# Kernel optimization log

Hardware: AMD Instinct MI355X
Metric: run time of the kernel (lower is better)

The kernel has to match this reference:

```python
import jax, jax.numpy as jnp
import numpy as np

B, H, W, C = 2, 64, 64, 96
DIN, NST, RNK, K = 192, 16, 6, 4
L = H * W


def _make_ids():
    idx = np.arange(L).reshape(H, W)
    p0 = idx.reshape(-1)
    p1 = idx.T.reshape(-1)
    p2 = p0[::-1].copy()
    p3 = p1[::-1].copy()
    scan = np.stack([p0, p1, p2, p3]).astype(np.int32)
    inv = np.stack([np.argsort(p) for p in scan]).astype(np.int32)
    return jnp.asarray(scan), jnp.asarray(inv)


def setup_inputs() -> dict:
    key = jax.random.key(0)
    ks = jax.random.split(key, 10)
    scan_ids, inv_ids = _make_ids()
    std = RNK ** -0.5
    # dt bias init: inverse-softplus of dt ~ LogUniform(1e-3, 1e-1), as in VMM.dt_init
    u = jax.random.uniform(ks[5], (K, DIN))
    dt = jnp.exp(u * (np.log(0.1) - np.log(0.001)) + np.log(0.001))
    dt_b = dt + jnp.log(-jnp.expm1(-dt))
    return {
        "x": jax.random.normal(ks[0], (B, H, W, C), jnp.float32),
        "W_in": jax.random.normal(ks[1], (2 * DIN, C), jnp.float32) * 0.02,
        "conv_w": jax.random.normal(ks[2], (DIN, 1, 3, 3), jnp.float32) * 0.1,
        "conv_b": jnp.zeros((DIN,), jnp.float32),
        "x_proj_w": jax.random.normal(ks[3], (K, RNK + 2 * NST, DIN), jnp.float32) * 0.02,
        "dt_w": jax.random.uniform(ks[4], (K, DIN, RNK), jnp.float32, -std, std),
        "dt_b": dt_b.astype(jnp.float32),
        "A_logs": jnp.log(jnp.tile(jnp.arange(1, NST + 1, dtype=jnp.float32)[None], (K * DIN, 1))),
        "Ds": jnp.ones((K * DIN,), jnp.float32),
        "gate_w": jax.random.normal(ks[6], (4 * DIN, 4), jnp.float32) * 0.1,  # grouped 1x1 conv, groups=DIN
        "gate_b": jnp.zeros((4 * DIN,), jnp.float32),
        "ln_g": jnp.ones((DIN,), jnp.float32),
        "ln_b": jnp.zeros((DIN,), jnp.float32),
        "W_out": jax.random.normal(ks[7], (C, DIN), jnp.float32) * 0.02,
        "scan_ids": scan_ids,
        "inv_ids": inv_ids,
    }


def _forward(x, W_in, conv_w, conv_b, x_proj_w, dt_w, dt_b, A_logs, Ds, gate_w, gate_b, ln_g, ln_b, W_out, scan_ids, inv_ids):
    b, h, w, c = x.shape
    l = h * w
    din = conv_w.shape[0]
    k = x_proj_w.shape[0]
    nst = A_logs.shape[1]
    rnk = dt_w.shape[2]
    # in_proj + split into x / gate z
    xz = x @ W_in.T
    xc, z = jnp.split(xz, 2, axis=-1)
    xc = jnp.transpose(xc, (0, 3, 1, 2))  # (b, din, h, w)
    # depthwise 3x3 conv + SiLU
    xc = jax.lax.conv_general_dilated(
        xc, conv_w, (1, 1), "SAME", feature_group_count=din,
        dimension_numbers=("NCHW", "OIHW", "NCHW")) + conv_b[None, :, None, None]
    xc = jax.nn.silu(xc)
    # multi-directional gather (mair_ids_scan)
    xf = xc.reshape(b, din, l)
    xs = jnp.moveaxis(xf[:, :, scan_ids], 2, 1)  # (b, k, din, l)
    # x_proj (grouped 1x1 conv) -> dt, B, C
    x_dbl = jnp.einsum("bkdl,krd->bkrl", xs, x_proj_w)
    dts, Bs, Cs = jnp.split(x_dbl, [rnk, rnk + nst], axis=2)  # (b,k,rnk,l),(b,k,n,l),(b,k,n,l)
    delta = jax.nn.softplus(jnp.einsum("bkrl,kdr->bkdl", dts, dt_w) + dt_b[None, :, :, None])
    A = -jnp.exp(A_logs).reshape(k, din, nst)
    dA = jnp.exp(delta[..., None] * A[None, :, :, None, :])              # (b,k,d,l,n)
    dBu = (delta * xs)[..., None] * jnp.moveaxis(Bs, 2, 3)[:, :, None]   # (b,k,d,l,n)

    def step(hst, inp):
        da, dbu = inp
        hst = da * hst + dbu
        return hst, hst

    h0 = jnp.zeros((b, k, din, nst), jnp.float32)
    _, hs = jax.lax.scan(step, h0, (jnp.moveaxis(dA, 3, 0), jnp.moveaxis(dBu, 3, 0)))  # (l,b,k,d,n)
    ys = jnp.einsum("lbkdn,bknl->bkdl", hs, Cs) + xs * Ds.reshape(k, din)[None, :, :, None]
    # inverse scatter (mair_ids_inverse) + concat along channels
    y = jax.vmap(lambda yk, ik: yk[..., ik], in_axes=(1, 0), out_axes=1)(ys, inv_ids)
    y = y.reshape(b, k * din, h, w)
    # ShuffleAttn gating: group = din, group_channels = k
    shuf = y.reshape(b, k, din, h, w).transpose(0, 2, 1, 3, 4).reshape(b, k * din, h, w)
    pooled = shuf.mean(axis=(2, 3)).reshape(b, din, k)
    gate = jax.nn.sigmoid(jnp.einsum("bgi,goi->bgo", pooled, gate_w.reshape(din, k, k)) + gate_b.reshape(din, k))
    gate = gate.transpose(0, 2, 1).reshape(b, k * din)  # channel_rearrange
    y = y * gate[:, :, None, None]
    # sum the 4 direction branches
    y = y.reshape(b, k, din, h, w).sum(axis=1)
    y = jnp.transpose(y, (0, 2, 3, 1))  # (b,h,w,din)
    # LayerNorm(d_inner)
    mu = y.mean(-1, keepdims=True)
    var = ((y - mu) ** 2).mean(-1, keepdims=True)
    y = (y - mu) / jnp.sqrt(var + 1e-5) * ln_g + ln_b
    y = y * jax.nn.silu(z)
    return y @ W_out.T


def reference(x, W_in, conv_w, conv_b, x_proj_w, dt_w, dt_b, A_logs, Ds, gate_w, gate_b, ln_g, ln_b, W_out, scan_ids, inv_ids):
    return _forward(x, W_in, conv_w, conv_b, x_proj_w, dt_w, dt_b, A_logs, Ds, gate_w, gate_b, ln_g, ln_b, W_out, scan_ids, inv_ids)
```

## Files before the change

kernel.cpp:

```cpp
#include <hip/hip_runtime.h>
#include <math.h>

#define BB 2
#define CC 96
#define DIN 192
#define NST 16
#define RNK 6
#define KK 4
#define LL 4096
#define RTOT (RNK + 2*NST)


__global__ __launch_bounds__(256) void k_inproj(const float* __restrict__ x,
        const float* __restrict__ W_in, float* __restrict__ xc_pre,
        float* __restrict__ z_silu) {
    __shared__ float lx[96*65];
    __shared__ float wt[48*196];
    int b = blockIdx.y;
    int l0 = blockIdx.x * 64;
    int t = threadIdx.x;
    for (int i = 0; i < 6; ++i) {
        int e4 = t + 256*i;
        int c4 = e4 % 24, l = e4 / 24;
        float4 v = *(const float4*)&x[((size_t)(b*LL + l0 + l))*96 + 4*c4];
        lx[(4*c4+0)*65 + l] = v.x;
        lx[(4*c4+1)*65 + l] = v.y;
        lx[(4*c4+2)*65 + l] = v.z;
        lx[(4*c4+3)*65 + l] = v.w;
    }
    int lg = t & 15;
    int og = t >> 4;
    for (int z = 0; z < 2; ++z) {
        float acc[4][12];
        #pragma unroll
        for (int j = 0; j < 4; ++j)
            #pragma unroll
            for (int q = 0; q < 12; ++q) acc[j][q] = 0.f;
        for (int p = 0; p < 2; ++p) {
            __syncthreads();
            for (int i = 0; i < 9; ++i) {
                int e4 = t + 256*i;
                int cc4 = e4 % 12, oc = e4 / 12;
                float4 v = *(const float4*)&W_in[((size_t)(z*192 + oc))*96 + p*48 + 4*cc4];
                wt[(4*cc4+0)*196 + oc] = v.x;
                wt[(4*cc4+1)*196 + oc] = v.y;
                wt[(4*cc4+2)*196 + oc] = v.z;
                wt[(4*cc4+3)*196 + oc] = v.w;
            }
            __syncthreads();
            #pragma unroll 2
            for (int cc = 0; cc < 48; ++cc) {
                int c = p*48 + cc;
                float x0 = lx[c*65 + 4*lg + 0];
                float x1 = lx[c*65 + 4*lg + 1];
                float x2 = lx[c*65 + 4*lg + 2];
                float x3 = lx[c*65 + 4*lg + 3];
                const float* wr = &wt[cc*196 + 12*og];
                float4 w0 = *(const float4*)(wr);
                float4 w1 = *(const float4*)(wr + 4);
                float4 w2 = *(const float4*)(wr + 8);
                float wv[12] = {w0.x,w0.y,w0.z,w0.w, w1.x,w1.y,w1.z,w1.w,
                                w2.x,w2.y,w2.z,w2.w};
                #pragma unroll
                for (int q = 0; q < 12; ++q) {
                    acc[0][q] += x0*wv[q];
                    acc[1][q] += x1*wv[q];
                    acc[2][q] += x2*wv[q];
                    acc[3][q] += x3*wv[q];
                }
            }
        }
        float* dst = (z == 0) ? xc_pre : z_silu;
        #pragma unroll
        for (int j = 0; j < 4; ++j) {
            int l = l0 + 4*lg + j;
            size_t base = (size_t)(b*LL + l)*DIN + 12*og;
            float v[12];
            #pragma unroll
            for (int q = 0; q < 12; ++q) {
                float a = acc[j][q];
                v[q] = z ? a/(1.f + __expf(-a)) : a;
            }
            *(float4*)&dst[base]     = make_float4(v[0],v[1],v[2],v[3]);
            *(float4*)&dst[base + 4] = make_float4(v[4],v[5],v[6],v[7]);
            *(float4*)&dst[base + 8] = make_float4(v[8],v[9],v[10],v[11]);
        }
    }
}

__global__ __launch_bounds__(256) void k_conv(const float* __restrict__ xc,
        const float* __restrict__ cw, const float* __restrict__ cb,
        float* __restrict__ out) {
    int gid = blockIdx.x*256 + threadIdx.x;
    int dq = gid % 48;
    int r = gid / 48;
    int l = r & 4095, b = r >> 12;
    int w = l & 63, h = l >> 6;
    int d0 = dq*4;
    float4 acc = *(const float4*)&cb[d0];
    float wreg[4][9];
    #pragma unroll
    for (int j = 0; j < 4; ++j)
        #pragma unroll
        for (int tp = 0; tp < 9; ++tp) wreg[j][tp] = cw[(d0+j)*9 + tp];
    #pragma unroll
    for (int dh = -1; dh <= 1; ++dh) {
        int h2 = h + dh;
        bool okh = (h2 >= 0) && (h2 < 64);
        #pragma unroll
        for (int dw = -1; dw <= 1; ++dw) {
            int w2 = w + dw;
            if (okh && w2 >= 0 && w2 < 64) {
                float4 v = *(const float4*)&xc[((size_t)(b*LL + h2*64 + w2))*DIN + d0];
                int tp = (dh+1)*3 + (dw+1);
                acc.x += v.x*wreg[0][tp];
                acc.y += v.y*wreg[1][tp];
                acc.z += v.z*wreg[2][tp];
                acc.w += v.w*wreg[3][tp];
            }
        }
    }
    float4 o;
    o.x = acc.x/(1.f + __expf(-acc.x));
    o.y = acc.y/(1.f + __expf(-acc.y));
    o.z = acc.z/(1.f + __expf(-acc.z));
    o.w = acc.w/(1.f + __expf(-acc.w));
    *(float4*)&out[((size_t)(b*LL + l))*DIN + d0] = o;
}

__global__ __launch_bounds__(512) void k_proj(const float* __restrict__ xconv,
        const int* __restrict__ scan_ids, const float* __restrict__ xpw,
        float* __restrict__ dts, float* __restrict__ Bs, float* __restrict__ Cs) {
    __shared__ float lxs[96*65];
    __shared__ float lw[RTOT*96];
    __shared__ float lbc[64*33];
    __shared__ int lsid[64];
    int k = blockIdx.y, b = blockIdx.z;
    int l0 = blockIdx.x * 64;
    int t = threadIdx.x;
    if (t < 64) lsid[t] = scan_ids[k*LL + l0 + t];
    int l = t & 63;
    int rg = __builtin_amdgcn_readfirstlane(t >> 6);
    float acc[5];
    #pragma unroll
    for (int j = 0; j < 5; ++j) acc[j] = 0.f;
    for (int p = 0; p < 2; ++p) {
        __syncthreads();
        for (int i = 0; i < 3; ++i) {
            int e4 = t + 512*i;
            int dd4 = e4 % 24, ll = e4 / 24;
            float4 v = *(const float4*)&xconv[((size_t)(b*LL + lsid[ll]))*DIN + p*96 + 4*dd4];
            lxs[(4*dd4+0)*65 + ll] = v.x;
            lxs[(4*dd4+1)*65 + ll] = v.y;
            lxs[(4*dd4+2)*65 + ll] = v.z;
            lxs[(4*dd4+3)*65 + ll] = v.w;
        }
        for (int i = 0; i < 2; ++i) {
            int e4 = t + 512*i;
            if (e4 < RTOT*24) {
                int r = e4 / 24, dd4 = e4 % 24;
                *(float4*)&lw[r*96 + 4*dd4] =
                    *(const float4*)&xpw[(size_t)k*RTOT*DIN + r*DIN + p*96 + 4*dd4];
            }
        }
        __syncthreads();
        for (int dd = 0; dd < 96; dd += 4) {
            float x0 = lxs[(dd+0)*65 + l];
            float x1 = lxs[(dd+1)*65 + l];
            float x2 = lxs[(dd+2)*65 + l];
            float x3 = lxs[(dd+3)*65 + l];
            #pragma unroll
            for (int j = 0; j < 5; ++j) {
                int r = rg + 8*j;
                if (r < RTOT) {
                    float4 w = *(const float4*)&lw[r*96 + dd];
                    acc[j] += x0*w.x + x1*w.y + x2*w.z + x3*w.w;
                }
            }
        }
    }
    int bk = b*KK + k;
    #pragma unroll
    for (int j = 0; j < 5; ++j) {
        int r = rg + 8*j;
        if (r < RNK)       dts[((size_t)bk*LL + l0 + l)*8 + r] = acc[j];
        else if (r < RTOT) lbc[l*33 + (r - RNK)] = acc[j];
    }
    __syncthreads();
    size_t rowb = ((size_t)bk*LL + l0)*NST;
    for (int i = 0; i < 2; ++i) {
        int e = t + 512*i;
        int n = e & 15, ll = e >> 4;
        Bs[rowb + ll*NST + n] = lbc[ll*33 + n];
        Cs[rowb + ll*NST + n] = lbc[ll*33 + 16 + n];
    }
}

__global__ __launch_bounds__(384) void k_scan1(const float* __restrict__ xconv,
        const float* __restrict__ Bs, const float* __restrict__ Cs,
        const float* __restrict__ dts, const float* __restrict__ dtw,
        const float* __restrict__ dtb,
        const int* __restrict__ scan_ids, const float* __restrict__ A_logs,
        const float* __restrict__ Ds,
        float* __restrict__ y_dirs, float* __restrict__ segA,
        float* __restrict__ segB, int SL) {
    int seg = blockIdx.x, bk = blockIdx.y;
    int b = bk >> 2, k = bk & 3;
    int t = threadIdx.x;
    int half = t & 1, d = t >> 1;
    int l0 = seg * SL;
    float Av[8];
    {
        const float4* ap = (const float4*)(A_logs + ((k*DIN + d)*NST + half*8));
        float4 a0 = ap[0], a1 = ap[1];
        Av[0]=-__expf(a0.x); Av[1]=-__expf(a0.y); Av[2]=-__expf(a0.z); Av[3]=-__expf(a0.w);
        Av[4]=-__expf(a1.x); Av[5]=-__expf(a1.y); Av[6]=-__expf(a1.z); Av[7]=-__expf(a1.w);
    }
    float Dv = Ds[k*DIN + d];
    float wdt[RNK];
    float bdt = dtb[k*DIN + d];
    #pragma unroll
    for (int r = 0; r < RNK; ++r) wdt[r] = dtw[(k*DIN + d)*RNK + r];
    float h[8];
    #pragma unroll
    for (int n = 0; n < 8; ++n) h[n] = 0.f;
    float sumdv = 0.f;
    const int* sid = scan_ids + k*LL + l0;
    const float* dbase = dts + ((size_t)bk*LL + l0)*8;
    const float* bbase = Bs + ((size_t)bk*LL + l0)*NST + half*8;
    const float* cbase = Cs + ((size_t)bk*LL + l0)*NST + half*8;
    int ln = sid[0];
    float xn = xconv[((size_t)(b*LL + ln))*DIN + d];
    float drc[RNK];
    #pragma unroll
    for (int r = 0; r < RNK; ++r) drc[r] = dbase[r];
    float4 bn0 = *(const float4*)bbase,      bn1 = *(const float4*)(bbase + 4);
    float4 cn0 = *(const float4*)cbase,      cn1 = *(const float4*)(cbase + 4);
    for (int li = 0; li < SL; ++li) {
        int l = ln;
        float xv = xn;
        float drv[RNK];
        #pragma unroll
        for (int r = 0; r < RNK; ++r) drv[r] = drc[r];
        float4 b0 = bn0, b1 = bn1, c0v = cn0, c1v = cn1;
        if (li + 1 < SL) {
            ln = sid[li + 1];
            xn = xconv[((size_t)(b*LL + ln))*DIN + d];
            #pragma unroll
            for (int r = 0; r < RNK; ++r) drc[r] = dbase[(li+1)*8 + r];
            bn0 = *(const float4*)(bbase + (size_t)(li+1)*NST);
            bn1 = *(const float4*)(bbase + (size_t)(li+1)*NST + 4);
            cn0 = *(const float4*)(cbase + (size_t)(li+1)*NST);
            cn1 = *(const float4*)(cbase + (size_t)(li+1)*NST + 4);
        }
        float aa = bdt;
        #pragma unroll
        for (int r = 0; r < RNK; ++r) aa += drv[r]*wdt[r];
        float dv = fmaxf(aa, 0.f) + __logf(1.f + __expf(-fabsf(aa)));
        sumdv += dv;
        float dxv = dv * xv;
        float bb[8] = {b0.x,b0.y,b0.z,b0.w, b1.x,b1.y,b1.z,b1.w};
        float cc[8] = {c0v.x,c0v.y,c0v.z,c0v.w, c1v.x,c1v.y,c1v.z,c1v.w};
        float y = 0.f;
        #pragma unroll
        for (int n = 0; n < 8; ++n) {
            float e2 = __expf(dv * Av[n]);
            h[n] = e2*h[n] + dxv*bb[n];
            y += h[n]*cc[n];
        }
        y += __shfl_xor(y, 1);
        if (half == 0) {
            y += xv * Dv;
            y_dirs[((size_t)(bk*LL + l))*DIN + d] = y;
        }
    }
    float a[8];
    #pragma unroll
    for (int n = 0; n < 8; ++n) a[n] = __expf(Av[n]*sumdv);
    size_t base = (((size_t)bk*gridDim.x + seg)*DIN + d)*NST + half*8;
    *(float4*)&segA[base]     = make_float4(a[0],a[1],a[2],a[3]);
    *(float4*)&segA[base + 4] = make_float4(a[4],a[5],a[6],a[7]);
    *(float4*)&segB[base]     = make_float4(h[0],h[1],h[2],h[3]);
    *(float4*)&segB[base + 4] = make_float4(h[4],h[5],h[6],h[7]);
}

__global__ __launch_bounds__(256) void k_scan2(const float* segA,
        const float* segB, float* hinit, int SEGC) {
    int idx = blockIdx.x*256 + threadIdx.x;
    if (idx >= BB*KK*DIN*NST) return;
    int bk = idx / (DIN*NST);
    int dn = idx % (DIN*NST);
    const size_t stride = DIN*NST;
    size_t o = (size_t)bk*SEGC*stride + dn;
    float h = 0.f;
    for (int s = 0; s < SEGC; s += 8) {
        float av[8], bv[8];
        #pragma unroll
        for (int j = 0; j < 8; ++j) {
            av[j] = segA[o + j*stride];
            bv[j] = segB[o + j*stride];
        }
        #pragma unroll
        for (int j = 0; j < 8; ++j) {
            hinit[o + j*stride] = h;
            h = av[j]*h + bv[j];
        }
        o += 8*stride;
    }
}

__global__ __launch_bounds__(384) void k_apply(const float* __restrict__ Cs,
        const float* __restrict__ dts, const float* __restrict__ dtw,
        const float* __restrict__ dtb,
        const int* __restrict__ scan_ids, const float* __restrict__ A_logs,
        const float* __restrict__ hinit,
        float* __restrict__ y_dirs, float* __restrict__ poolsum, int SL) {
    int seg = blockIdx.x, bk = blockIdx.y;
    int b = bk >> 2, k = bk & 3;
    int t = threadIdx.x;
    int half = t & 1, d = t >> 1;
    int l0 = seg * SL;
    float Av[8];
    {
        const float4* ap = (const float4*)(A_logs + ((k*DIN + d)*NST + half*8));
        float4 a0 = ap[0], a1 = ap[1];
        Av[0]=-__expf(a0.x); Av[1]=-__expf(a0.y); Av[2]=-__expf(a0.z); Av[3]=-__expf(a0.w);
        Av[4]=-__expf(a1.x); Av[5]=-__expf(a1.y); Av[6]=-__expf(a1.z); Av[7]=-__expf(a1.w);
    }
    float Av0 = -__expf(A_logs[(k*DIN + d)*NST]);
    bool okl = true;
    #pragma unroll
    for (int q = 0; q < 8; ++q) {
        float m = (float)(half*8 + q + 1);
        okl = okl && (fabsf(Av[q] - m*Av0) <= 1e-4f*m);
    }
    int fast = __all(okl);
    float h0[8];
    {
        size_t base = (((size_t)bk*gridDim.x + seg)*DIN + d)*NST + half*8;
        float4 v0 = *(const float4*)&hinit[base];
        float4 v1 = *(const float4*)&hinit[base + 4];
        h0[0]=v0.x; h0[1]=v0.y; h0[2]=v0.z; h0[3]=v0.w;
        h0[4]=v1.x; h0[5]=v1.y; h0[6]=v1.z; h0[7]=v1.w;
    }
    float wdt[RNK];
    float bdt = dtb[k*DIN + d];
    #pragma unroll
    for (int r = 0; r < RNK; ++r) wdt[r] = dtw[(k*DIN + d)*RNK + r];
    float cum = 0.f;
    float pool = 0.f;
    const int* sid = scan_ids + k*LL + l0;
    const float* dbase = dts + ((size_t)bk*LL + l0)*8;
    const float* cbase = Cs + ((size_t)bk*LL + l0)*NST + half*8;
    float drc[RNK];
    #pragma unroll
    for (int r = 0; r < RNK; ++r) drc[r] = dbase[r];
    float4 cn0 = *(const float4*)cbase, cn1 = *(const float4*)(cbase + 4);
    for (int li = 0; li < SL; ++li) {
        int l = sid[li];
        float drv[RNK];
        #pragma unroll
        for (int r = 0; r < RNK; ++r) drv[r] = drc[r];
        float4 c0v = cn0, c1v = cn1;
        if (li + 1 < SL) {
            #pragma unroll
            for (int r = 0; r < RNK; ++r) drc[r] = dbase[(li+1)*8 + r];
            cn0 = *(const float4*)(cbase + (size_t)(li+1)*NST);
            cn1 = *(const float4*)(cbase + (size_t)(li+1)*NST + 4);
        }
        float aa = bdt;
        #pragma unroll
        for (int r = 0; r < RNK; ++r) aa += drv[r]*wdt[r];
        cum += fmaxf(aa, 0.f) + __logf(1.f + __expf(-fabsf(aa)));
        float cc[8] = {c0v.x,c0v.y,c0v.z,c0v.w, c1v.x,c1v.y,c1v.z,c1v.w};
        float g;
        if (fast) {
            float E = __expf(Av0 * cum);
            g = 0.f;
            #pragma unroll
            for (int q = 7; q >= 0; --q) g = g*E + cc[q]*h0[q];
            g *= E;
            if (half) {
                float E2 = E*E, E4 = E2*E2;
                g *= E4*E4;
            }
        } else {
            g = 0.f;
            #pragma unroll
            for (int q = 0; q < 8; ++q)
                g += cc[q]*h0[q]*__expf(Av[q]*cum);
        }
        g += __shfl_xor(g, 1);
        if (half == 0) {
            size_t yo = ((size_t)(bk*LL + l))*DIN + d;
            float y = y_dirs[yo] + g;
            y_dirs[yo] = y;
            pool += y;
        }
    }
    if (half == 0) atomicAdd(&poolsum[(b*DIN + d)*KK + k], pool);
}

__global__ __launch_bounds__(256) void k_final(const float* __restrict__ y_dirs,
        const float* __restrict__ poolsum, const float* __restrict__ gw,
        const float* __restrict__ gb, const float* __restrict__ z_silu,
        const float* __restrict__ lng, const float* __restrict__ lnb,
        const float* __restrict__ Wout, float* __restrict__ out) {
    __shared__ float buf[16*196];
    __shared__ float lgate[DIN*KK];
    __shared__ float lmu[16], lrs[16];
    int b = blockIdx.y;
    int l0 = blockIdx.x * 16;
    int t = threadIdx.x;
    for (int e = t; e < DIN*KK; e += 256) {
        int d = e >> 2, o = e & 3;
        float acc = gb[d*KK + o];
        #pragma unroll
        for (int i = 0; i < KK; ++i)
            acc += (poolsum[(b*DIN + d)*KK + i] * (1.f/LL)) * gw[(d*KK + o)*KK + i];
        lgate[d*KK + o] = 1.f/(1.f + __expf(-acc));
    }
    __syncthreads();
    for (int i = 0; i < 3; ++i) {
        int e4 = t + 256*i;
        int d4 = e4 % 48, l = e4 / 48;
        int db = 4*d4;
        float4 acc = make_float4(0.f, 0.f, 0.f, 0.f);
        #pragma unroll
        for (int k = 0; k < KK; ++k) {
            float4 v = *(const float4*)&y_dirs[((size_t)((b*KK + k)*LL + l0 + l))*DIN + db];
            acc.x += v.x * lgate[(db+0)*KK + k];
            acc.y += v.y * lgate[(db+1)*KK + k];
            acc.z += v.z * lgate[(db+2)*KK + k];
            acc.w += v.w * lgate[(db+3)*KK + k];
        }
        *(float4*)&buf[l*196 + db] = acc;
    }
    __syncthreads();
    int l2 = t >> 4, q = t & 15;
    float s = 0.f, s2 = 0.f;
    for (int i = 0; i < 12; ++i) {
        float v = buf[l2*196 + q + 16*i];
        s += v; s2 += v*v;
    }
    s += __shfl_xor(s, 1);  s2 += __shfl_xor(s2, 1);
    s += __shfl_xor(s, 2);  s2 += __shfl_xor(s2, 2);
    s += __shfl_xor(s, 4);  s2 += __shfl_xor(s2, 4);
    s += __shfl_xor(s, 8);  s2 += __shfl_xor(s2, 8);
    if (q == 0) {
        float mu = s * (1.f/DIN);
        float var = s2 * (1.f/DIN) - mu*mu;
        lmu[l2] = mu;
        lrs[l2] = rsqrtf(var + 1e-5f);
    }
    __syncthreads();
    for (int i = 0; i < 3; ++i) {
        int e4 = t + 256*i;
        int d4 = e4 % 48, l = e4 / 48;
        int db = 4*d4;
        float4 v  = *(float4*)&buf[l*196 + db];
        float4 g4 = *(const float4*)&lng[db];
        float4 b4 = *(const float4*)&lnb[db];
        float4 z4 = *(const float4*)&z_silu[((size_t)(b*LL + l0 + l))*DIN + db];
        float mu = lmu[l], rs = lrs[l];
        v.x = ((v.x - mu)*rs*g4.x + b4.x) * z4.x;
        v.y = ((v.y - mu)*rs*g4.y + b4.y) * z4.y;
        v.z = ((v.z - mu)*rs*g4.z + b4.z) * z4.z;
        v.w = ((v.w - mu)*rs*g4.w + b4.w) * z4.w;
        *(float4*)&buf[l*196 + db] = v;
    }
    __syncthreads();
    int l = t & 15;
    int c0 = (t >> 4) * 6;
    float acc[6];
    #pragma unroll
    for (int cc = 0; cc < 6; ++cc) acc[cc] = 0.f;
    for (int d4 = 0; d4 < 48; ++d4) {
        float4 v = *(float4*)&buf[l*196 + 4*d4];
        #pragma unroll
        for (int cc = 0; cc < 6; ++cc) {
            float4 w = *(const float4*)&Wout[(c0 + cc)*DIN + 4*d4];
            acc[cc] += v.x*w.x + v.y*w.y + v.z*w.z + v.w*w.w;
        }
    }
    #pragma unroll
    for (int cc = 0; cc < 6; ++cc)
        out[((size_t)(b*LL + l0 + l))*CC + c0 + cc] = acc[cc];
}

extern "C" void kernel_launch(void* const* d_in, const int* in_sizes, int n_in,
                              void* d_out, int out_size, void* d_ws, size_t ws_size,
                              hipStream_t stream) {
    const float* x      = (const float*)d_in[0];
    const float* W_in   = (const float*)d_in[1];
    const float* conv_w = (const float*)d_in[2];
    const float* conv_b = (const float*)d_in[3];
    const float* xpw    = (const float*)d_in[4];
    const float* dt_w   = (const float*)d_in[5];
    const float* dt_b   = (const float*)d_in[6];
    const float* A_logs = (const float*)d_in[7];
    const float* Ds     = (const float*)d_in[8];
    const float* gate_w = (const float*)d_in[9];
    const float* gate_b = (const float*)d_in[10];
    const float* ln_g   = (const float*)d_in[11];
    const float* ln_b   = (const float*)d_in[12];
    const float* W_out  = (const float*)d_in[13];
    const int* scan_ids = (const int*)d_in[14];
    float* out = (float*)d_out;

    const size_t baseF = 6291456ull + 2ull*1572864 + 262144ull + 2ull*524288 + 3072;
    int SEGC = 16;
    if ((baseF + 2ull*128*24576)*4 <= ws_size) SEGC = 128;
    else if ((baseF + 2ull*64*24576)*4 <= ws_size) SEGC = 64;
    else if ((baseF + 2ull*32*24576)*4 <= ws_size) SEGC = 32;
    int SL = LL / SEGC;
    size_t segF = (size_t)SEGC * 24576;

    float* ws      = (float*)d_ws;
    float* y_dirs  = ws;
    float* xc_pre  = ws;
    float* z_silu  = y_dirs  + 6291456;
    float* xconv   = z_silu  + 1572864;
    float* dts     = xconv   + 1572864;
    float* Bs      = dts     + 262144;
    float* Cs      = Bs      + 524288;
    float* poolsum = Cs      + 524288;
    float* segA    = poolsum + 3072;
    float* segB    = segA    + segF;
    float* hinit   = segA;

    hipMemsetAsync(poolsum, 0, 1536*sizeof(float), stream);

    k_inproj<<<dim3(LL/64, BB), 256, 0, stream>>>(x, W_in, xc_pre, z_silu);
    k_conv<<<(BB*LL*48)/256, 256, 0, stream>>>(xc_pre, conv_w, conv_b, xconv);
    k_proj<<<dim3(LL/64, KK, BB), 512, 0, stream>>>(xconv, scan_ids, xpw,
                                                    dts, Bs, Cs);
    k_scan1<<<dim3(SEGC, BB*KK), 384, 0, stream>>>(xconv, Bs, Cs, dts, dt_w, dt_b,
                                                   scan_ids, A_logs, Ds,
                                                   y_dirs, segA, segB, SL);
    k_scan2<<<(BB*KK*DIN*NST + 255)/256, 256, 0, stream>>>(segA, segB, hinit, SEGC);
    k_apply<<<dim3(SEGC, BB*KK), 384, 0, stream>>>(Cs, dts, dt_w, dt_b,
                                                   scan_ids, A_logs, hinit,
                                                   y_dirs, poolsum, SL);
    k_final<<<dim3(LL/16, BB), 256, 0, stream>>>(y_dirs, poolsum, gate_w, gate_b,
                                                 z_silu, ln_g, ln_b, W_out, out);
}
```

Before: 286.7 us.

## Split in_proj over more blocks, stage W_out in LDS, fold poolsum zeroing

The input projection now launches a separate block per output half (x vs z) and per 32 tokens, giving four times as many blocks with fewer accumulators per thread. The final kernel stages W_out through shared memory in two chunks instead of reading it from global memory per thread. The poolsum memset is removed and done inside k_scan2, saving one stream operation. In exchange, x is reloaded by more blocks, W_in is reloaded more often, and k_final's shared memory grows, which may lower its occupancy.

```diff
diff --git a/kernel.cpp b/kernel.cpp
--- a/kernel.cpp
+++ b/kernel.cpp
@@ -14,77 +14,74 @@
 __global__ __launch_bounds__(256) void k_inproj(const float* __restrict__ x,
         const float* __restrict__ W_in, float* __restrict__ xc_pre,
         float* __restrict__ z_silu) {
-    __shared__ float lx[96*65];
+    __shared__ float lx[96*33];
     __shared__ float wt[48*196];
-    int b = blockIdx.y;
-    int l0 = blockIdx.x * 64;
+    int b = blockIdx.y, z = blockIdx.z;
+    int l0 = blockIdx.x * 32;
     int t = threadIdx.x;
-    for (int i = 0; i < 6; ++i) {
+    for (int i = 0; i < 3; ++i) {
         int e4 = t + 256*i;
         int c4 = e4 % 24, l = e4 / 24;
         float4 v = *(const float4*)&x[((size_t)(b*LL + l0 + l))*96 + 4*c4];
-        lx[(4*c4+0)*65 + l] = v.x;
-        lx[(4*c4+1)*65 + l] = v.y;
-        lx[(4*c4+2)*65 + l] = v.z;
-        lx[(4*c4+3)*65 + l] = v.w;
-    }
-    int lg = t & 15;
-    int og = t >> 4;
-    for (int z = 0; z < 2; ++z) {
-        float acc[4][12];
-        #pragma unroll
-        for (int j = 0; j < 4; ++j)
-            #pragma unroll
-            for (int q = 0; q < 12; ++q) acc[j][q] = 0.f;
-        for (int p = 0; p < 2; ++p) {
-            __syncthreads();
-            for (int i = 0; i < 9; ++i) {
-                int e4 = t + 256*i;
-                int cc4 = e4 % 12, oc = e4 / 12;
-                float4 v = *(const float4*)&W_in[((size_t)(z*192 + oc))*96 + p*48 + 4*cc4];
-                wt[(4*cc4+0)*196 + oc] = v.x;
-                wt[(4*cc4+1)*196 + oc] = v.y;
-                wt[(4*cc4+2)*196 + oc] = v.z;
-                wt[(4*cc4+3)*196 + oc] = v.w;
+        lx[(4*c4+0)*33 + l] = v.x;
+        lx[(4*c4+1)*33 + l] = v.y;
+        lx[(4*c4+2)*33 + l] = v.z;
+        lx[(4*c4+3)*33 + l] = v.w;
+    }
+    int lg = t & 7;
+    int og = t >> 3;
+    float acc[4][6];
+    #pragma unroll
+    for (int j = 0; j < 4; ++j)
+        #pragma unroll
+        for (int q = 0; q < 6; ++q) acc[j][q] = 0.f;
+    for (int p = 0; p < 2; ++p) {
+        __syncthreads();
+        for (int i = 0; i < 9; ++i) {
+            int e4 = t + 256*i;
+            int cc4 = e4 % 12, oc = e4 / 12;
+            float4 v = *(const float4*)&W_in[((size_t)(z*192 + oc))*96 + p*48 + 4*cc4];
+            wt[(4*cc4+0)*196 + oc] = v.x;
+            wt[(4*cc4+1)*196 + oc] = v.y;
+            wt[(4*cc4+2)*196 + oc] = v.z;
+            wt[(4*cc4+3)*196 + oc] = v.w;
+        }
+        __syncthreads();
+        #pragma unroll 4
+        for (int cc = 0; cc < 48; ++cc) {
+            int c = p*48 + cc;
+            float x0 = lx[c*33 + 4*lg + 0];
+            float x1 = lx[c*33 + 4*lg + 1];
+            float x2 = lx[c*33 + 4*lg + 2];
+            float x3 = lx[c*33 + 4*lg + 3];
+            const float* wr = &wt[cc*196 + 6*og];
+            float2 w0 = *(const float2*)(wr);
+            float2 w1 = *(const float2*)(wr + 2);
+            float2 w2 = *(const float2*)(wr + 4);
+            float wv[6] = {w0.x,w0.y, w1.x,w1.y, w2.x,w2.y};
+            #pragma unroll
+            for (int q = 0; q < 6; ++q) {
+                acc[0][q] += x0*wv[q];
+                acc[1][q] += x1*wv[q];
+                acc[2][q] += x2*wv[q];
+                acc[3][q] += x3*wv[q];
             }
-            __syncthreads();
-            #pragma unroll 2
-            for (int cc = 0; cc < 48; ++cc) {
-                int c = p*48 + cc;
-                float x0 = lx[c*65 + 4*lg + 0];
-                float x1 = lx[c*65 + 4*lg + 1];
-                float x2 = lx[c*65 + 4*lg + 2];
-                float x3 = lx[c*65 + 4*lg + 3];
-                const float* wr = &wt[cc*196 + 12*og];
-                float4 w0 = *(const float4*)(wr);
-                float4 w1 = *(const float4*)(wr + 4);
-                float4 w2 = *(const float4*)(wr + 8);
-                float wv[12] = {w0.x,w0.y,w0.z,w0.w, w1.x,w1.y,w1.z,w1.w,
-                                w2.x,w2.y,w2.z,w2.w};
-                #pragma unroll
-                for (int q = 0; q < 12; ++q) {
-                    acc[0][q] += x0*wv[q];
-                    acc[1][q] += x1*wv[q];
-                    acc[2][q] += x2*wv[q];
-                    acc[3][q] += x3*wv[q];
-                }
-            }
-        }
-        float* dst = (z == 0) ? xc_pre : z_silu;
-        #pragma unroll
-        for (int j = 0; j < 4; ++j) {
-            int l = l0 + 4*lg + j;
-            size_t base = (size_t)(b*LL + l)*DIN + 12*og;
-            float v[12];
-            #pragma unroll
-            for (int q = 0; q < 12; ++q) {
-                float a = acc[j][q];
-                v[q] = z ? a/(1.f + __expf(-a)) : a;
-            }
-            *(float4*)&dst[base]     = make_float4(v[0],v[1],v[2],v[3]);
-            *(float4*)&dst[base + 4] = make_float4(v[4],v[5],v[6],v[7]);
-            *(float4*)&dst[base + 8] = make_float4(v[8],v[9],v[10],v[11]);
-        }
+        }
+    }
+    float* dst = (z == 0) ? xc_pre : z_silu;
+    #pragma unroll
+    for (int j = 0; j < 4; ++j) {
+        int l = l0 + 4*lg + j;
+        size_t base = (size_t)(b*LL + l)*DIN + 6*og;
+        float v[6];
+        #pragma unroll
+        for (int q = 0; q < 6; ++q) {
+            float a = acc[j][q];
+            v[q] = z ? a/(1.f + __expf(-a)) : a;
+        }
+        *(float2*)&dst[base]     = make_float2(v[0], v[1]);
+        *(float2*)&dst[base + 2] = make_float2(v[2], v[3]);
+        *(float2*)&dst[base + 4] = make_float2(v[4], v[5]);
     }
 }
 
@@ -285,8 +282,9 @@
 }
 
 __global__ __launch_bounds__(256) void k_scan2(const float* segA,
-        const float* segB, float* hinit, int SEGC) {
+        const float* segB, float* hinit, float* poolsum, int SEGC) {
     int idx = blockIdx.x*256 + threadIdx.x;
+    if (idx < BB*DIN*KK) poolsum[idx] = 0.f;
     if (idx >= BB*KK*DIN*NST) return;
     int bk = idx / (DIN*NST);
     int dn = idx % (DIN*NST);
@@ -408,6 +406,7 @@
         const float* __restrict__ Wout, float* __restrict__ out) {
     __shared__ float buf[16*196];
     __shared__ float lgate[DIN*KK];
+    __shared__ float lwout[96*100];
     __shared__ float lmu[16], lrs[16];
     int b = blockIdx.y;
     int l0 = blockIdx.x * 16;
@@ -469,18 +468,27 @@
         v.w = ((v.w - mu)*rs*g4.w + b4.w) * z4.w;
         *(float4*)&buf[l*196 + db] = v;
     }
-    __syncthreads();
     int l = t & 15;
     int c0 = (t >> 4) * 6;
     float acc[6];
     #pragma unroll
     for (int cc = 0; cc < 6; ++cc) acc[cc] = 0.f;
-    for (int d4 = 0; d4 < 48; ++d4) {
-        float4 v = *(float4*)&buf[l*196 + 4*d4];
-        #pragma unroll
-        for (int cc = 0; cc < 6; ++cc) {
-            float4 w = *(const float4*)&Wout[(c0 + cc)*DIN + 4*d4];
-            acc[cc] += v.x*w.x + v.y*w.y + v.z*w.z + v.w*w.w;
+    for (int p = 0; p < 2; ++p) {
+        __syncthreads();
+        for (int i = 0; i < 9; ++i) {
+            int e4 = t + 256*i;
+            int dd4 = e4 % 24, cc = e4 / 24;
+            *(float4*)&lwout[cc*100 + 4*dd4] =
+                *(const float4*)&Wout[(size_t)cc*DIN + p*96 + 4*dd4];
+        }
+        __syncthreads();
+        for (int d4 = 0; d4 < 24; ++d4) {
+            float4 v = *(float4*)&buf[l*196 + p*96 + 4*d4];
+            #pragma unroll
+            for (int cc = 0; cc < 6; ++cc) {
+                float4 w = *(const float4*)&lwout[(c0 + cc)*100 + 4*d4];
+                acc[cc] += v.x*w.x + v.y*w.y + v.z*w.z + v.w*w.w;
+            }
         }
     }
     #pragma unroll
@@ -529,16 +537,15 @@
     float* segB    = segA    + segF;
     float* hinit   = segA;
 
-    hipMemsetAsync(poolsum, 0, 1536*sizeof(float), stream);
-
-    k_inproj<<<dim3(LL/64, BB), 256, 0, stream>>>(x, W_in, xc_pre, z_silu);
+    k_inproj<<<dim3(LL/32, BB, 2), 256, 0, stream>>>(x, W_in, xc_pre, z_silu);
     k_conv<<<(BB*LL*48)/256, 256, 0, stream>>>(xc_pre, conv_w, conv_b, xconv);
     k_proj<<<dim3(LL/64, KK, BB), 512, 0, stream>>>(xconv, scan_ids, xpw,
                                                     dts, Bs, Cs);
     k_scan1<<<dim3(SEGC, BB*KK), 384, 0, stream>>>(xconv, Bs, Cs, dts, dt_w, dt_b,
                                                    scan_ids, A_logs, Ds,
                                                    y_dirs, segA, segB, SL);
-    k_scan2<<<(BB*KK*DIN*NST + 255)/256, 256, 0, stream>>>(segA, segB, hinit, SEGC);
+    k_scan2<<<(BB*KK*DIN*NST + 255)/256, 256, 0, stream>>>(segA, segB, hinit,
+                                                           poolsum, SEGC);
     k_apply<<<dim3(SEGC, BB*KK), 384, 0, stream>>>(Cs, dts, dt_w, dt_b,
                                                    scan_ids, A_logs, hinit,
                                                    y_dirs, poolsum, SL);
```

Measured after the change: 272.6 us. 4.9% less time.
